# Kernel tuning notes

Measured on AMD Instinct MI355X. Metric: run time of the kernel, lower is better.

Reference implementation:

```python
import jax, jax.numpy as jnp
import numpy as np

B, S, D_IN, D_OUT = 8, 2048, 1024, 1024

def setup_inputs() -> dict:
    key = jax.random.key(0)
    ks = jax.random.split(key, 6)
    return {
        "inputs_for_keys": jax.random.normal(ks[0], (B, S, D_IN), dtype=jnp.float32),
        "inputs_for_values": jax.random.normal(ks[1], (B, S, D_IN), dtype=jnp.float32),
        "inputs_for_queries": jax.random.normal(ks[2], (B, S, D_IN), dtype=jnp.float32),
        "W_K": jax.random.normal(ks[3], (D_IN, D_OUT), dtype=jnp.float32) * 0.05,
        "W_V": jax.random.normal(ks[4], (D_IN, D_OUT), dtype=jnp.float32) * 0.05,
        "W_Q": jax.random.normal(ks[5], (D_IN, D_OUT), dtype=jnp.float32) * 0.05,
    }

def reference(inputs_for_keys, inputs_for_values, inputs_for_queries, W_K, W_V, W_Q):
    # Linear projections: [B,S,D_in] @ [D_in,D_out] -> [B,S,D_out]
    K = jnp.einsum("bsd,de->bse", inputs_for_keys, W_K)
    V = jnp.einsum("bsd,de->bse", inputs_for_values, W_V)
    Q = jnp.einsum("bsd,de->bse", inputs_for_queries, W_Q)
    scale = jnp.sqrt(jnp.asarray(K.shape[-1], dtype=K.dtype))
    # Scaled dot-product attention scores: [B,Sq,Sk]
    scores = jnp.einsum("bqe,bke->bqk", Q, K) / scale
    probs = jax.nn.softmax(scores, axis=-1)
    Z = jnp.einsum("bqk,bke->bqe", probs, V)
    return Z
```

## Files before the change

### kernel.cpp

```cpp
#include <hip/hip_runtime.h>
#include <hip/hip_bf16.h>
#include <stdint.h>

#define BATCH 8
#define SEQ 2048
#define DMODEL 1024

typedef __attribute__((ext_vector_type(4))) float f32x4;
typedef __attribute__((ext_vector_type(8))) short bf16x8;
typedef __attribute__((ext_vector_type(4))) uint32_t u32x4;
typedef __attribute__((ext_vector_type(2))) uint32_t u32x2;

#define MFMA16(a, b, c) __builtin_amdgcn_mfma_f32_16x16x32_bf16((a), (b), (c), 0, 0, 0)


static __device__ __forceinline__ uint16_t f2bf(float f) {
    uint32_t u = __builtin_bit_cast(uint32_t, f);
    u += 0x7fffu + ((u >> 16) & 1u);
    return (uint16_t)(u >> 16);
}
static __device__ __forceinline__ uint32_t pk2(float lo, float hi) {
    return (uint32_t)f2bf(lo) | ((uint32_t)f2bf(hi) << 16);
}
static __device__ __forceinline__ void gload16(const uint16_t* g, uint16_t* l) {
    __builtin_amdgcn_global_load_lds((const __attribute__((address_space(1))) void*)g,
                                     (__attribute__((address_space(3))) void*)l, 16, 0, 0);
}

__global__ __launch_bounds__(256) void cast3_bf16_pk(const float* __restrict__ x0,
                                                     const float* __restrict__ x1,
                                                     const float* __restrict__ x2,
                                                     uint16_t* __restrict__ d0,
                                                     uint16_t* __restrict__ d1,
                                                     uint16_t* __restrict__ d2) {
    const int z = blockIdx.y;
    const float* src = z == 0 ? x0 : (z == 1 ? x1 : x2);
    uint16_t* dst = z == 0 ? d0 : (z == 1 ? d1 : d2);
    const size_t c = (size_t)blockIdx.x * 256 + threadIdx.x;
    const size_t panel = c >> 11;
    const int w = (int)(c & 2047);
    const int ks = w >> 4, r15 = w & 15;
    const float* s = src + (panel * 16 + r15) * DMODEL + ks * 8;
    f32x4 a = *(const f32x4*)s;
    f32x4 b = *(const f32x4*)(s + 4);
    u32x4 o = {pk2(a[0], a[1]), pk2(a[2], a[3]), pk2(b[0], b[1]), pk2(b[2], b[3])};
    *(u32x4*)(dst + c * 8) = o;
}

__global__ void wt_cast_kernel(const float* __restrict__ Wk, const float* __restrict__ Wv,
                               const float* __restrict__ Wq, uint16_t* __restrict__ WT) {
    const float* W = blockIdx.z == 0 ? Wk : (blockIdx.z == 1 ? Wv : Wq);
    uint16_t* dst = WT + (size_t)blockIdx.z * DMODEL * DMODEL;
    __shared__ float tile[32][33];
    const int x = blockIdx.x * 32, y = blockIdx.y * 32;
    const int tx = threadIdx.x, ty = threadIdx.y;
#pragma unroll
    for (int j = 0; j < 4; j++)
        tile[ty * 4 + j][tx] = W[(size_t)(y + ty * 4 + j) * DMODEL + x + tx];
    __syncthreads();
#pragma unroll
    for (int j = 0; j < 4; j++) {
        const int n = x + ty * 4 + j, k = y + tx;
        const size_t off = ((size_t)(n >> 4) * (DMODEL / 8) + (k >> 3)) * 128 +
                           (n & 15) * 8 + (k & 7);
        dst[off] = f2bf(tile[tx][ty * 4 + j]);
    }
}

#define STG_A(kt, sl, h)                                                          \
    do {                                                                          \
        const size_t g0 = (size_t)((h) * 8 + (tid >> 7)) * eldA +                 \
                          (size_t)(kt) * 1024 + (tid & 127) * 8;                  \
        gload16(Ab + g0, &As[sl][(h) * 8192 + tid * 8]);                          \
        gload16(Ab + g0 + 4 * eldA, &As[sl][(h) * 8192 + tid * 8 + 4096]);        \
    } while (0)
#define STG_B(kt, sl, h)                                                          \
    do {                                                                          \
        const size_t g0 = (size_t)((h) * 8 + (tid >> 7)) * eldB +                 \
                          (size_t)(kt) * 1024 + (tid & 127) * 8;                  \
        gload16(Bb + g0, &Bs[sl][(h) * 8192 + tid * 8]);                          \
        gload16(Bb + g0 + 4 * eldB, &Bs[sl][(h) * 8192 + tid * 8 + 4096]);        \
    } while (0)

#define READ_B(sl)                                                                \
    _Pragma("unroll") for (int j = 0; j < 4; j++) {                               \
        bfr[j][0] = *(const bf16x8*)&Bs[sl][(wc * 4 + j) * 1024 + lbase];         \
        bfr[j][1] = *(const bf16x8*)&Bs[sl][(wc * 4 + j) * 1024 + 512 + lbase];   \
    }

#define VM4 asm volatile("s_waitcnt vmcnt(4)" ::: "memory")
#define VM0 asm volatile("s_waitcnt vmcnt(0)" ::: "memory")
#define NOPW (void)0
#define NOST (void)0

#define MFMA_Q(q)                                                                 \
    __builtin_amdgcn_s_setprio(1);                                                \
    _Pragma("unroll") for (int j = 0; j < 4; j++) {                               \
        acc[2 * (q)][j] = MFMA16(a00, bfr[j][0], acc[2 * (q)][j]);                \
        acc[2 * (q)][j] = MFMA16(a01, bfr[j][1], acc[2 * (q)][j]);                \
        acc[2 * (q) + 1][j] = MFMA16(a10, bfr[j][0], acc[2 * (q) + 1][j]);        \
        acc[2 * (q) + 1][j] = MFMA16(a11, bfr[j][1], acc[2 * (q) + 1][j]);        \
    }                                                                             \
    __builtin_amdgcn_s_setprio(0);

#define PH_FREE(sl, q, STG)                                                       \
    do {                                                                          \
        const int ab = (wr * 8 + 2 * (q)) * 1024 + lbase;                         \
        bf16x8 a00 = *(const bf16x8*)&As[sl][ab];                                 \
        bf16x8 a01 = *(const bf16x8*)&As[sl][ab + 512];                           \
        bf16x8 a10 = *(const bf16x8*)&As[sl][ab + 1024];                          \
        bf16x8 a11 = *(const bf16x8*)&As[sl][ab + 1536];                          \
        STG;                                                                      \
        asm volatile("s_waitcnt lgkmcnt(0)" ::: "memory");                        \
        __builtin_amdgcn_sched_barrier(0);                                        \
        MFMA_Q(q)                                                                 \
    } while (0)

#define PH_SYNC(sl, q, STG, WAIT)                                                 \
    do {                                                                          \
        const int ab = (wr * 8 + 2 * (q)) * 1024 + lbase;                         \
        bf16x8 a00 = *(const bf16x8*)&As[sl][ab];                                 \
        bf16x8 a01 = *(const bf16x8*)&As[sl][ab + 512];                           \
        bf16x8 a10 = *(const bf16x8*)&As[sl][ab + 1024];                          \
        bf16x8 a11 = *(const bf16x8*)&As[sl][ab + 1536];                          \
        STG;                                                                      \
        WAIT;                                                                     \
        __builtin_amdgcn_s_barrier();                                             \
        asm volatile("s_waitcnt lgkmcnt(0)" ::: "memory");                        \
        __builtin_amdgcn_sched_barrier(0);                                        \
        MFMA_Q(q)                                                                 \
        __builtin_amdgcn_s_barrier();                                             \
    } while (0)

template <int MODE, int BX>
__global__ __launch_bounds__(512, 2) void gemm8p(const uint16_t* __restrict__ Ag,
                                                 const uint16_t* __restrict__ Bg,
                                                 void* __restrict__ Cg,
                                                 const float* __restrict__ Linv,
                                                 float scale, int lda, int ldb, int ldc,
                                                 int nk, size_t sA, size_t sB, size_t sC,
                                                 const uint16_t* __restrict__ A2,
                                                 const uint16_t* __restrict__ A3,
                                                 void* __restrict__ C2,
                                                 void* __restrict__ C3) {
    __shared__ __align__(16) uint16_t As[3][16384];
    __shared__ __align__(16) uint16_t Bs[2][16384];
    const int bz = BX ? blockIdx.x : blockIdx.z;
    const int bm = BX ? blockIdx.y : blockIdx.x;
    const int bn = BX ? blockIdx.z : blockIdx.y;
    const int m0 = bm * 256, n0 = bn * 256;
    const uint16_t *Abase, *Bbase;
    if constexpr (MODE == 3) {
        Abase = (bz == 0) ? Ag : (bz == 1) ? A2 : A3;
        Bbase = Bg + ((bz == 0) ? 2 * sB : (bz == 1) ? (size_t)0 : sB);
    } else {
        Abase = Ag + (size_t)bz * sA;
        Bbase = Bg + (size_t)bz * sB;
    }
    const uint16_t* Ab = Abase + (size_t)m0 * lda;
    const uint16_t* Bb = Bbase + (size_t)n0 * ldb;
    const int tid = threadIdx.x, lane = tid & 63;
    const int wid = tid >> 6, wr = wid >> 2, wc = wid & 3;
    const int lr = lane & 15, lg = lane >> 4;
    const int lbase = lg * 128 + lr * 8;
    const size_t eldA = (size_t)lda * 16, eldB = (size_t)ldb * 16;

    f32x4 acc[8][4] = {};
    bf16x8 bfr[4][2];
    STG_A(0, 0, 0); STG_A(0, 0, 1);
    STG_B(0, 0, 0); STG_B(0, 0, 1);
    STG_A(1, 1, 0); STG_A(1, 1, 1);
    VM4;
    __builtin_amdgcn_s_barrier();
    int sa = 0, sa2 = 2, sb = 0;
    for (int kt = 0; kt < nk - 2; ++kt) {
        READ_B(sb);
        PH_FREE(sa, 0, STG_B(kt + 1, sb ^ 1, 0));
        PH_FREE(sa, 1, STG_B(kt + 1, sb ^ 1, 1));
        PH_FREE(sa, 2, STG_A(kt + 2, sa2, 0));
        PH_SYNC(sa, 3, STG_A(kt + 2, sa2, 1), VM4);
        sa = (sa == 2) ? 0 : sa + 1;
        sa2 = (sa2 == 2) ? 0 : sa2 + 1;
        sb ^= 1;
    }
    READ_B(sb);
    PH_FREE(sa, 0, STG_B(nk - 1, sb ^ 1, 0));
    PH_FREE(sa, 1, STG_B(nk - 1, sb ^ 1, 1));
    PH_FREE(sa, 2, NOST);
    PH_SYNC(sa, 3, NOST, VM0);
    sa = (sa == 2) ? 0 : sa + 1;
    sb ^= 1;
    READ_B(sb);
    PH_FREE(sa, 0, NOST);
    PH_FREE(sa, 1, NOST);
    PH_FREE(sa, 2, NOST);
    PH_SYNC(sa, 3, NOST, NOPW);

    if constexpr (MODE == 0) {
        uint16_t* C = (uint16_t*)Cg + (size_t)bz * sC;
#pragma unroll
        for (int i = 0; i < 8; i++) {
            const int gm = m0 + wr * 128 + i * 16 + lg * 4;
            const size_t pbase = (size_t)(gm >> 4) * (ldc / 8);
#pragma unroll
            for (int j = 0; j < 4; j++) {
                const int gn = n0 + wc * 64 + j * 16 + lr;
                const size_t off = (pbase + (gn >> 3)) * 128 + (gn & 7);
#pragma unroll
                for (int r = 0; r < 4; r++)
                    C[off + (lg * 4 + r) * 8] = f2bf(acc[i][j][r] * scale);
            }
        }
    } else if constexpr (MODE == 1) {
        uint16_t* C = (uint16_t*)Cg;
#pragma unroll
        for (int i = 0; i < 8; i++) {
            const int gm = m0 + wr * 128 + i * 16 + lg * 4;
            const int bb = gm / SEQ;
            const int s0 = gm - bb * SEQ;
            uint16_t* Cb = C + (size_t)bb * DMODEL * SEQ;
#pragma unroll
            for (int j = 0; j < 4; j++) {
                const int e = n0 + wc * 64 + j * 16 + lr;
                const size_t off = ((size_t)(e >> 4) * (SEQ / 8) + (s0 >> 3)) * 128 +
                                   (e & 15) * 8 + (s0 & 7);
                u32x2 v = {pk2(acc[i][j][0], acc[i][j][1]), pk2(acc[i][j][2], acc[i][j][3])};
                *(u32x2*)&Cb[off] = v;
            }
        }
    } else if constexpr (MODE == 2) {
        float* C = (float*)Cg + (size_t)bz * sC;
        const float* LB = Linv + bz * SEQ;
#pragma unroll
        for (int i = 0; i < 8; i++) {
            const int gm = m0 + wr * 128 + i * 16 + lg * 4;
            const f32x4 lv = *(const f32x4*)&LB[gm];
#pragma unroll
            for (int j = 0; j < 4; j++) {
                const int gn = n0 + wc * 64 + j * 16 + lr;
#pragma unroll
                for (int r = 0; r < 4; r++)
                    C[(size_t)(gm + r) * ldc + gn] = acc[i][j][r] * lv[r];
            }
        }
    } else {
        if (bz < 2) {
            uint16_t* C = (uint16_t*)(bz == 0 ? Cg : C2);
            const float sc = bz == 0 ? scale : 1.0f;
#pragma unroll
            for (int i = 0; i < 8; i++) {
                const int gm = m0 + wr * 128 + i * 16 + lg * 4;
                const size_t pbase = (size_t)(gm >> 4) * (ldc / 8);
#pragma unroll
                for (int j = 0; j < 4; j++) {
                    const int gn = n0 + wc * 64 + j * 16 + lr;
                    const size_t off = (pbase + (gn >> 3)) * 128 + (gn & 7);
#pragma unroll
                    for (int r = 0; r < 4; r++)
                        C[off + (lg * 4 + r) * 8] = f2bf(acc[i][j][r] * sc);
                }
            }
        } else {
            uint16_t* C = (uint16_t*)C3;
#pragma unroll
            for (int i = 0; i < 8; i++) {
                const int gm = m0 + wr * 128 + i * 16 + lg * 4;
                const int bb = gm / SEQ;
                const int s0 = gm - bb * SEQ;
                uint16_t* Cb = C + (size_t)bb * DMODEL * SEQ;
#pragma unroll
                for (int j = 0; j < 4; j++) {
                    const int e = n0 + wc * 64 + j * 16 + lr;
                    const size_t off = ((size_t)(e >> 4) * (SEQ / 8) + (s0 >> 3)) * 128 +
                                       (e & 15) * 8 + (s0 & 7);
                    u32x2 v = {pk2(acc[i][j][0], acc[i][j][1]),
                               pk2(acc[i][j][2], acc[i][j][3])};
                    *(u32x2*)&Cb[off] = v;
                }
            }
        }
    }
}

__global__ __launch_bounds__(256) void softmax_pk(uint16_t* __restrict__ S,
                                                  float* __restrict__ Linv) {
    const size_t panel = blockIdx.x;
    uint16_t* sp = S + panel * (size_t)(16 * SEQ);
    const int t = threadIdx.x, lane = t & 63, w = t >> 6;
    const int r15 = t & 15, ksl = t >> 4;
    __shared__ float rm[4][16], rs[4][16];
    u32x4 raw[16];
    float mx = -3.0e38f;
#pragma unroll
    for (int u = 0; u < 16; u++) {
        raw[u] = *(const u32x4*)&sp[(ksl + u * 16) * 128 + r15 * 8];
#pragma unroll
        for (int j = 0; j < 4; j++) {
            mx = fmaxf(mx, __builtin_bit_cast(float, raw[u][j] << 16));
            mx = fmaxf(mx, __builtin_bit_cast(float, raw[u][j] & 0xffff0000u));
        }
    }
    mx = fmaxf(mx, __shfl_xor(mx, 16));
    mx = fmaxf(mx, __shfl_xor(mx, 32));
    if (lane < 16) rm[w][lane] = mx;
    __syncthreads();
    const float m = fmaxf(fmaxf(rm[0][r15], rm[1][r15]), fmaxf(rm[2][r15], rm[3][r15]));
    float sum = 0.0f;
#pragma unroll
    for (int u = 0; u < 16; u++) {
#pragma unroll
        for (int j = 0; j < 4; j++) {
            float lo = __expf(__builtin_bit_cast(float, raw[u][j] << 16) - m);
            float hi = __expf(__builtin_bit_cast(float, raw[u][j] & 0xffff0000u) - m);
            sum += lo + hi;
            raw[u][j] = pk2(lo, hi);
        }
    }
    sum += __shfl_xor(sum, 16);
    sum += __shfl_xor(sum, 32);
    if (lane < 16) rs[w][lane] = sum;
    __syncthreads();
    const float tot = rs[0][r15] + rs[1][r15] + rs[2][r15] + rs[3][r15];
#pragma unroll
    for (int u = 0; u < 16; u++)
        *(u32x4*)&sp[(ksl + u * 16) * 128 + r15 * 8] = raw[u];
    if (w == 0 && lane < 16) Linv[panel * 16 + lane] = 1.0f / tot;
}

extern "C" void kernel_launch(void* const* d_in, const int* in_sizes, int n_in,
                              void* d_out, int out_size, void* d_ws, size_t ws_size,
                              hipStream_t stream) {
    const float* Xk = (const float*)d_in[0];
    const float* Xv = (const float*)d_in[1];
    const float* Xq = (const float*)d_in[2];
    const float* Wk = (const float*)d_in[3];
    const float* Wv = (const float*)d_in[4];
    const float* Wq = (const float*)d_in[5];
    float* out = (float*)d_out;
    char* ws = (char*)d_ws;
    uint16_t* Qbf = (uint16_t*)(ws);
    uint16_t* Kbf = (uint16_t*)(ws + (size_t)33554432);
    uint16_t* VTb = (uint16_t*)(ws + (size_t)67108864);
    uint16_t* WT  = (uint16_t*)(ws + (size_t)100663296);
    float*    Linv= (float*)(ws + (size_t)106954752);
    uint16_t* Sb  = (uint16_t*)(ws + (size_t)107020288);
    uint16_t* XqB = (uint16_t*)d_out;
    uint16_t* XkB = Sb;
    uint16_t* XvB = (uint16_t*)(ws + (size_t)140574720);

    wt_cast_kernel<<<dim3(32, 32, 3), dim3(32, 8), 0, stream>>>(Wk, Wv, Wq, WT);
    cast3_bf16_pk<<<dim3(8192, 3), 256, 0, stream>>>(Xq, Xk, Xv, XqB, XkB, XvB);
    gemm8p<3, 0><<<dim3(64, 4, 3), 512, 0, stream>>>(
        XqB, WT, (void*)Qbf, nullptr, 0.03125f,
        DMODEL, DMODEL, DMODEL, DMODEL / 64,
        0, (size_t)1048576 , 0,
        XkB, XvB, (void*)Kbf, (void*)VTb);
    gemm8p<0, 1><<<dim3(8, 8, 8), 512, 0, stream>>>(
        Qbf, Kbf, (void*)Sb, nullptr, 1.0f,
        DMODEL, DMODEL, SEQ, DMODEL / 64,
        (size_t)SEQ * DMODEL, (size_t)SEQ * DMODEL, (size_t)SEQ * SEQ,
        nullptr, nullptr, nullptr, nullptr);
    softmax_pk<<<dim3(BATCH * SEQ / 16), 256, 0, stream>>>(Sb, Linv);
    gemm8p<2, 1><<<dim3(8, 8, 4), 512, 0, stream>>>(
        Sb, VTb, (void*)out, Linv, 1.0f,
        SEQ, SEQ, DMODEL, SEQ / 64,
        (size_t)SEQ * SEQ, (size_t)DMODEL * SEQ, (size_t)SEQ * DMODEL,
        nullptr, nullptr, nullptr, nullptr);
}
```

Baseline: 342.7 us.

## Switch GEMM inner loop from 16x16x32 to 32x32x16 bf16 MFMA

Replaces the 16x16x32 MFMA tiling with 32x32x16 MFMA instructions. Each wave now holds 4x2 32x32 accumulator tiles, and the LDS fragment loads and all epilogue index mappings are remapped to the 32x32 output layout. The larger instruction reuses each A/B fragment across more output and needs fewer LDS reads per FLOP, which is meant to raise MFMA throughput. The risks are a wrong lane mapping against the packed LDS layout, and different register pressure and latency behaviour.

```diff
diff --git a/kernel.cpp b/kernel.cpp
--- a/kernel.cpp
+++ b/kernel.cpp
@@ -7,11 +7,12 @@
 #define DMODEL 1024
 
 typedef __attribute__((ext_vector_type(4))) float f32x4;
+typedef __attribute__((ext_vector_type(16))) float f32x16;
 typedef __attribute__((ext_vector_type(8))) short bf16x8;
 typedef __attribute__((ext_vector_type(4))) uint32_t u32x4;
 typedef __attribute__((ext_vector_type(2))) uint32_t u32x2;
 
-#define MFMA16(a, b, c) __builtin_amdgcn_mfma_f32_16x16x32_bf16((a), (b), (c), 0, 0, 0)
+#define MFMA32(a, b, c) __builtin_amdgcn_mfma_f32_32x32x16_bf16((a), (b), (c), 0, 0, 0)
 
 
 static __device__ __forceinline__ uint16_t f2bf(float f) {
@@ -83,10 +84,10 @@
     } while (0)
 
 #define READ_B(sl)                                                                \
-    _Pragma("unroll") for (int j = 0; j < 4; j++) {                               \
-        bfr[j][0] = *(const bf16x8*)&Bs[sl][(wc * 4 + j) * 1024 + lbase];         \
-        bfr[j][1] = *(const bf16x8*)&Bs[sl][(wc * 4 + j) * 1024 + 512 + lbase];   \
-    }
+    _Pragma("unroll") for (int ct = 0; ct < 2; ct++)                              \
+        _Pragma("unroll") for (int ks = 0; ks < 4; ks++)                          \
+            bfr[ct][ks] = *(const bf16x8*)&Bs[sl][(wc * 4 + ct * 2) * 1024 +      \
+                                                  lb32 + ks * 256];
 
 #define VM4 asm volatile("s_waitcnt vmcnt(4)" ::: "memory")
 #define VM0 asm volatile("s_waitcnt vmcnt(0)" ::: "memory")
@@ -95,21 +96,18 @@
 
 #define MFMA_Q(q)                                                                 \
     __builtin_amdgcn_s_setprio(1);                                                \
-    _Pragma("unroll") for (int j = 0; j < 4; j++) {                               \
-        acc[2 * (q)][j] = MFMA16(a00, bfr[j][0], acc[2 * (q)][j]);                \
-        acc[2 * (q)][j] = MFMA16(a01, bfr[j][1], acc[2 * (q)][j]);                \
-        acc[2 * (q) + 1][j] = MFMA16(a10, bfr[j][0], acc[2 * (q) + 1][j]);        \
-        acc[2 * (q) + 1][j] = MFMA16(a11, bfr[j][1], acc[2 * (q) + 1][j]);        \
+    _Pragma("unroll") for (int rt = 0; rt < 4; rt++) {                            \
+        acc[rt][0] = MFMA32(afr[rt], bfr[0][q], acc[rt][0]);                      \
+        acc[rt][1] = MFMA32(afr[rt], bfr[1][q], acc[rt][1]);                      \
     }                                                                             \
     __builtin_amdgcn_s_setprio(0);
 
 #define PH_FREE(sl, q, STG)                                                       \
     do {                                                                          \
-        const int ab = (wr * 8 + 2 * (q)) * 1024 + lbase;                         \
-        bf16x8 a00 = *(const bf16x8*)&As[sl][ab];                                 \
-        bf16x8 a01 = *(const bf16x8*)&As[sl][ab + 512];                           \
-        bf16x8 a10 = *(const bf16x8*)&As[sl][ab + 1024];                          \
-        bf16x8 a11 = *(const bf16x8*)&As[sl][ab + 1536];                          \
+        bf16x8 afr[4];                                                            \
+        _Pragma("unroll") for (int rt = 0; rt < 4; rt++)                          \
+            afr[rt] = *(const bf16x8*)&As[sl][(wr * 8 + rt * 2) * 1024 +          \
+                                              lb32 + (q) * 256];                  \
         STG;                                                                      \
         asm volatile("s_waitcnt lgkmcnt(0)" ::: "memory");                        \
         __builtin_amdgcn_sched_barrier(0);                                        \
@@ -118,11 +116,10 @@
 
 #define PH_SYNC(sl, q, STG, WAIT)                                                 \
     do {                                                                          \
-        const int ab = (wr * 8 + 2 * (q)) * 1024 + lbase;                         \
-        bf16x8 a00 = *(const bf16x8*)&As[sl][ab];                                 \
-        bf16x8 a01 = *(const bf16x8*)&As[sl][ab + 512];                           \
-        bf16x8 a10 = *(const bf16x8*)&As[sl][ab + 1024];                          \
-        bf16x8 a11 = *(const bf16x8*)&As[sl][ab + 1536];                          \
+        bf16x8 afr[4];                                                            \
+        _Pragma("unroll") for (int rt = 0; rt < 4; rt++)                          \
+            afr[rt] = *(const bf16x8*)&As[sl][(wr * 8 + rt * 2) * 1024 +          \
+                                              lb32 + (q) * 256];                  \
         STG;                                                                      \
         WAIT;                                                                     \
         __builtin_amdgcn_s_barrier();                                             \
@@ -161,12 +158,13 @@
     const uint16_t* Bb = Bbase + (size_t)n0 * ldb;
     const int tid = threadIdx.x, lane = tid & 63;
     const int wid = tid >> 6, wr = wid >> 2, wc = wid & 3;
-    const int lr = lane & 15, lg = lane >> 4;
-    const int lbase = lg * 128 + lr * 8;
+    const int lb32 = ((lane >> 4) & 1) * 1024 + (lane >> 5) * 128 + (lane & 15) * 8;
+    const int hv = lane >> 5;
+    const int cl = lane & 31;
     const size_t eldA = (size_t)lda * 16, eldB = (size_t)ldb * 16;
 
-    f32x4 acc[8][4] = {};
-    bf16x8 bfr[4][2];
+    f32x16 acc[4][2] = {};
+    bf16x8 bfr[2][4];
     STG_A(0, 0, 0); STG_A(0, 0, 1);
     STG_B(0, 0, 0); STG_B(0, 0, 1);
     STG_A(1, 1, 0); STG_A(1, 1, 1);
@@ -199,85 +197,91 @@
     if constexpr (MODE == 0) {
         uint16_t* C = (uint16_t*)Cg + (size_t)bz * sC;
 #pragma unroll
-        for (int i = 0; i < 8; i++) {
-            const int gm = m0 + wr * 128 + i * 16 + lg * 4;
-            const size_t pbase = (size_t)(gm >> 4) * (ldc / 8);
-#pragma unroll
-            for (int j = 0; j < 4; j++) {
-                const int gn = n0 + wc * 64 + j * 16 + lr;
-                const size_t off = (pbase + (gn >> 3)) * 128 + (gn & 7);
-#pragma unroll
-                for (int r = 0; r < 4; r++)
-                    C[off + (lg * 4 + r) * 8] = f2bf(acc[i][j][r] * scale);
-            }
-        }
+        for (int rt = 0; rt < 4; rt++)
+#pragma unroll
+            for (int ct = 0; ct < 2; ct++)
+#pragma unroll
+                for (int g = 0; g < 4; g++) {
+                    const int gm = m0 + wr * 128 + rt * 32 + g * 8 + hv * 4;
+                    const int gn = n0 + wc * 64 + ct * 32 + cl;
+                    const size_t off = ((size_t)(gm >> 4) * (ldc / 8) + (gn >> 3)) * 128 +
+                                       (gm & 15) * 8 + (gn & 7);
+#pragma unroll
+                    for (int r = 0; r < 4; r++)
+                        C[off + r * 8] = f2bf(acc[rt][ct][g * 4 + r] * scale);
+                }
     } else if constexpr (MODE == 1) {
         uint16_t* C = (uint16_t*)Cg;
 #pragma unroll
-        for (int i = 0; i < 8; i++) {
-            const int gm = m0 + wr * 128 + i * 16 + lg * 4;
-            const int bb = gm / SEQ;
-            const int s0 = gm - bb * SEQ;
-            uint16_t* Cb = C + (size_t)bb * DMODEL * SEQ;
-#pragma unroll
-            for (int j = 0; j < 4; j++) {
-                const int e = n0 + wc * 64 + j * 16 + lr;
-                const size_t off = ((size_t)(e >> 4) * (SEQ / 8) + (s0 >> 3)) * 128 +
-                                   (e & 15) * 8 + (s0 & 7);
-                u32x2 v = {pk2(acc[i][j][0], acc[i][j][1]), pk2(acc[i][j][2], acc[i][j][3])};
-                *(u32x2*)&Cb[off] = v;
-            }
-        }
+        for (int rt = 0; rt < 4; rt++)
+#pragma unroll
+            for (int ct = 0; ct < 2; ct++)
+#pragma unroll
+                for (int g = 0; g < 4; g++) {
+                    const int gm = m0 + wr * 128 + rt * 32 + g * 8 + hv * 4;
+                    const int bb = gm / SEQ;
+                    const int s0 = gm - bb * SEQ;
+                    const int e = n0 + wc * 64 + ct * 32 + cl;
+                    uint16_t* Cb = C + (size_t)bb * DMODEL * SEQ;
+                    const size_t off = ((size_t)(e >> 4) * (SEQ / 8) + (s0 >> 3)) * 128 +
+                                       (e & 15) * 8 + (s0 & 7);
+                    u32x2 v = {pk2(acc[rt][ct][g * 4], acc[rt][ct][g * 4 + 1]),
+                               pk2(acc[rt][ct][g * 4 + 2], acc[rt][ct][g * 4 + 3])};
+                    *(u32x2*)&Cb[off] = v;
+                }
     } else if constexpr (MODE == 2) {
         float* C = (float*)Cg + (size_t)bz * sC;
         const float* LB = Linv + bz * SEQ;
 #pragma unroll
-        for (int i = 0; i < 8; i++) {
-            const int gm = m0 + wr * 128 + i * 16 + lg * 4;
-            const f32x4 lv = *(const f32x4*)&LB[gm];
-#pragma unroll
-            for (int j = 0; j < 4; j++) {
-                const int gn = n0 + wc * 64 + j * 16 + lr;
-#pragma unroll
-                for (int r = 0; r < 4; r++)
-                    C[(size_t)(gm + r) * ldc + gn] = acc[i][j][r] * lv[r];
-            }
-        }
+        for (int rt = 0; rt < 4; rt++)
+#pragma unroll
+            for (int ct = 0; ct < 2; ct++)
+#pragma unroll
+                for (int g = 0; g < 4; g++) {
+                    const int gm = m0 + wr * 128 + rt * 32 + g * 8 + hv * 4;
+                    const int gn = n0 + wc * 64 + ct * 32 + cl;
+                    const f32x4 lv = *(const f32x4*)&LB[gm];
+#pragma unroll
+                    for (int r = 0; r < 4; r++)
+                        C[(size_t)(gm + r) * ldc + gn] = acc[rt][ct][g * 4 + r] * lv[r];
+                }
     } else {
         if (bz < 2) {
             uint16_t* C = (uint16_t*)(bz == 0 ? Cg : C2);
             const float sc = bz == 0 ? scale : 1.0f;
 #pragma unroll
-            for (int i = 0; i < 8; i++) {
-                const int gm = m0 + wr * 128 + i * 16 + lg * 4;
-                const size_t pbase = (size_t)(gm >> 4) * (ldc / 8);
-#pragma unroll
-                for (int j = 0; j < 4; j++) {
-                    const int gn = n0 + wc * 64 + j * 16 + lr;
-                    const size_t off = (pbase + (gn >> 3)) * 128 + (gn & 7);
-#pragma unroll
-                    for (int r = 0; r < 4; r++)
-                        C[off + (lg * 4 + r) * 8] = f2bf(acc[i][j][r] * sc);
-                }
-            }
+            for (int rt = 0; rt < 4; rt++)
+#pragma unroll
+                for (int ct = 0; ct < 2; ct++)
+#pragma unroll
+                    for (int g = 0; g < 4; g++) {
+                        const int gm = m0 + wr * 128 + rt * 32 + g * 8 + hv * 4;
+                        const int gn = n0 + wc * 64 + ct * 32 + cl;
+                        const size_t off = ((size_t)(gm >> 4) * (ldc / 8) + (gn >> 3)) * 128 +
+                                           (gm & 15) * 8 + (gn & 7);
+#pragma unroll
+                        for (int r = 0; r < 4; r++)
+                            C[off + r * 8] = f2bf(acc[rt][ct][g * 4 + r] * sc);
+                    }
         } else {
             uint16_t* C = (uint16_t*)C3;
 #pragma unroll
-            for (int i = 0; i < 8; i++) {
-                const int gm = m0 + wr * 128 + i * 16 + lg * 4;
-                const int bb = gm / SEQ;
-                const int s0 = gm - bb * SEQ;
-                uint16_t* Cb = C + (size_t)bb * DMODEL * SEQ;
-#pragma unroll
-                for (int j = 0; j < 4; j++) {
-                    const int e = n0 + wc * 64 + j * 16 + lr;
-                    const size_t off = ((size_t)(e >> 4) * (SEQ / 8) + (s0 >> 3)) * 128 +
-                                       (e & 15) * 8 + (s0 & 7);
-                    u32x2 v = {pk2(acc[i][j][0], acc[i][j][1]),
-                               pk2(acc[i][j][2], acc[i][j][3])};
-                    *(u32x2*)&Cb[off] = v;
-                }
-            }
+            for (int rt = 0; rt < 4; rt++)
+#pragma unroll
+                for (int ct = 0; ct < 2; ct++)
+#pragma unroll
+                    for (int g = 0; g < 4; g++) {
+                        const int gm = m0 + wr * 128 + rt * 32 + g * 8 + hv * 4;
+                        const int bb = gm / SEQ;
+                        const int s0 = gm - bb * SEQ;
+                        const int e = n0 + wc * 64 + ct * 32 + cl;
+                        uint16_t* Cb = C + (size_t)bb * DMODEL * SEQ;
+                        const size_t off = ((size_t)(e >> 4) * (SEQ / 8) + (s0 >> 3)) * 128 +
+                                           (e & 15) * 8 + (s0 & 7);
+                        u32x2 v = {pk2(acc[rt][ct][g * 4], acc[rt][ct][g * 4 + 1]),
+                                   pk2(acc[rt][ct][g * 4 + 2], acc[rt][ct][g * 4 + 3])};
+                        *(u32x2*)&Cb[off] = v;
+                    }
         }
     }
 }
```

Result: slower. 366.3 us (+6.9%).
